# Optimization experiments

Hardware: AMD Instinct MI355X
Metric: run time of the kernel (lower is better)

## Reference

```python
import jax, jax.numpy as jnp
import numpy as np

N = 100000      # nodes
E = 1600000     # edges (avg degree 16)
IN = 256        # in_dim
OUT = 64        # out_dim per head
H = 4           # num_heads
SLOPE = 0.01    # F.leaky_relu default negative_slope


def setup_inputs() -> dict:
    key = jax.random.key(0)
    k1, k2, k3, k4, k5 = jax.random.split(key, 5)
    h = jax.random.normal(k1, (N, IN), dtype=jnp.float32)
    # per-head projection Linear(in_dim, out_dim, bias=False): weight [OUT, IN]
    W = jax.random.normal(k2, (H, OUT, IN), dtype=jnp.float32) * (1.0 / np.sqrt(IN))
    # per-head attention Linear(2*out_dim, 1, bias=False): weight flattened to [2*OUT]
    attn = jax.random.normal(k3, (H, 2 * OUT), dtype=jnp.float32) * (1.0 / np.sqrt(2 * OUT))
    edge_src = jax.random.randint(k4, (E,), 0, N, dtype=jnp.int32)
    edge_dst = jax.random.randint(k5, (E,), 0, N, dtype=jnp.int32)
    return {"h": h, "W": W, "attn": attn, "edge_src": edge_src, "edge_dst": edge_dst}


def reference(h, W, attn, edge_src, edge_dst):
    # Bug-faithful: edge_attention always uses self.heads[0][1], i.e. head 0's
    # attention vector, for every head.
    a0 = attn[0]                      # [2*OUT]
    a_src, a_dst = a0[:OUT], a0[OUT:]
    outs = []
    for hd in range(H):               # fixed small structural loop over heads
        z = h @ W[hd].T               # [N, OUT]
        # concat(z_src, z_dst) @ a0 == z_src @ a_src + z_dst @ a_dst
        s_src = z @ a_src             # [N]
        s_dst = z @ a_dst             # [N]
        e = jax.nn.leaky_relu(s_src[edge_src] + s_dst[edge_dst], SLOPE)  # [E]
        # segment softmax over incoming edges of each destination node
        m = jax.ops.segment_max(e, edge_dst, num_segments=N)
        m = jnp.where(jnp.isfinite(m), m, 0.0)   # guard zero-in-degree nodes
        ex = jnp.exp(e - m[edge_dst])
        den = jax.ops.segment_sum(ex, edge_dst, num_segments=N)
        alpha = ex / jnp.maximum(den[edge_dst], 1e-9)          # [E]
        msg = alpha[:, None] * z[edge_src]                      # [E, OUT]
        outs.append(jax.ops.segment_sum(msg, edge_dst, num_segments=N))  # [N, OUT]
    return jnp.concatenate(outs, axis=1)  # merge='cat' -> [N, H*OUT]
```

## Files before the change

kernel.cpp:

```cpp
#include <hip/hip_runtime.h>

#define K_IN   256
#define C_OUT  256
#define HEADS  4
#define PAD    64
#define BKT    256
#define REP    16
#define CAP    448

typedef __attribute__((ext_vector_type(8))) short s16x8;
typedef __attribute__((ext_vector_type(4))) short s16x4;
typedef __attribute__((ext_vector_type(4))) float f32x4;
typedef __attribute__((ext_vector_type(4))) int   i32x4;

static __device__ __forceinline__ unsigned short f2bf(float f) {
  union { float f; unsigned u; } v; v.f = f;
  unsigned r = v.u + 0x7FFFu + ((v.u >> 16) & 1u);
  return (unsigned short)(r >> 16);
}
static __device__ __forceinline__ float bf2f(unsigned short u) {
  union { unsigned u; float f; } v; v.u = (unsigned)u << 16;
  return v.f;
}
static __device__ __forceinline__ unsigned cvt_pk_bf16(float lo, float hi) {
  unsigned r;
  asm volatile("v_cvt_pk_bf16_f32 %0, %1, %2" : "=v"(r) : "v"(lo), "v"(hi));
  return r;
}
static __device__ __forceinline__ float fast_exp2(float x) {
  float r;
  asm("v_exp_f32 %0, %1" : "=v"(r) : "v"(x));
  return r;
}

__global__ void cvt_w(const float* __restrict__ Wm, unsigned short* __restrict__ Wf) {
  int idx = blockIdx.x * blockDim.x + threadIdx.x;
  if (idx >= 65536) return;
  int j    = idx & 7;
  int lane = (idx >> 3) & 63;
  int s    = (idx >> 9) & 3;
  int ks   = (idx >> 11) & 7;
  int cb   = (idx >> 14) & 3;
  int c = cb * 64 + s * 16 + (lane & 15);
  int k = ks * 32 + (lane >> 4) * 8 + j;
  Wf[idx] = f2bf(Wm[c * K_IN + k]);
}

static __device__ __forceinline__ void gemm_body(int bid,
    const float* __restrict__ h, const unsigned short* __restrict__ Wf,
    const float* __restrict__ attn, unsigned short* __restrict__ zb,
    float* __restrict__ ssrc, float* __restrict__ sdst, int n_nodes) {
  const int wv   = threadIdx.x >> 6;
  const int lane = threadIdx.x & 63;
  const int l15  = lane & 15;
  const int lhi  = lane >> 4;
  const int r0   = bid * 64 + wv * 16;

  f32x4 acc[16];
#pragma unroll
  for (int f = 0; f < 16; ++f) acc[f] = (f32x4){0.f, 0.f, 0.f, 0.f};

  int n = r0 + l15;
  if (n > n_nodes - 1) n = n_nodes - 1;
  const long long arow = (long long)n * K_IN;
  const int kbase = lhi * 8;

#pragma unroll
  for (int ks = 0; ks < 8; ++ks) {
    const int k = ks * 32 + kbase;
    const float4* pa = reinterpret_cast<const float4*>(h + arow + k);
    float4 v0 = pa[0], v1 = pa[1];
    union { s16x8 v; unsigned u[4]; } au;
    au.u[0] = cvt_pk_bf16(v0.x, v0.y);
    au.u[1] = cvt_pk_bf16(v0.z, v0.w);
    au.u[2] = cvt_pk_bf16(v1.x, v1.y);
    au.u[3] = cvt_pk_bf16(v1.z, v1.w);
    s16x8 a = au.v;
#pragma unroll
    for (int f = 0; f < 16; ++f) {
      s16x8 b = *reinterpret_cast<const s16x8*>(
          Wf + (((f >> 2) * 8 + ks) * 4 + (f & 3)) * 512 + lane * 8);
      acc[f] = __builtin_amdgcn_mfma_f32_16x16x32_bf16(a, b, acc[f], 0, 0, 0);
    }
  }

#pragma unroll
  for (int reg = 0; reg < 4; ++reg) {
    int row = r0 + lhi * 4 + reg;
    if (row < n_nodes) {
#pragma unroll
      for (int f = 0; f < 16; ++f)
        zb[(size_t)row * C_OUT + f * 16 + l15] = f2bf(acc[f][reg]);
    }
  }

  const float LOG2E = 1.4426950408889634f;
  float as_[4], ad_[4];
#pragma unroll
  for (int s = 0; s < 4; ++s) {
    as_[s] = attn[s * 16 + l15];
    ad_[s] = attn[64 + s * 16 + l15];
  }
#pragma unroll
  for (int reg = 0; reg < 4; ++reg) {
    int row = r0 + lhi * 4 + reg;
    float ps[4], pd[4];
#pragma unroll
    for (int hd = 0; hd < 4; ++hd) {
      ps[hd] = acc[hd * 4 + 0][reg] * as_[0] + acc[hd * 4 + 1][reg] * as_[1] +
               acc[hd * 4 + 2][reg] * as_[2] + acc[hd * 4 + 3][reg] * as_[3];
      pd[hd] = acc[hd * 4 + 0][reg] * ad_[0] + acc[hd * 4 + 1][reg] * ad_[1] +
               acc[hd * 4 + 2][reg] * ad_[2] + acc[hd * 4 + 3][reg] * ad_[3];
#pragma unroll
      for (int d = 1; d < 16; d <<= 1) {
        ps[hd] += __shfl_xor(ps[hd], d, 64);
        pd[hd] += __shfl_xor(pd[hd], d, 64);
      }
    }
    if (l15 == 0 && row < n_nodes) {
#pragma unroll
      for (int hd = 0; hd < 4; ++hd) {
        ssrc[(size_t)row * 4 + hd] = ps[hd] * LOG2E;
        sdst[(size_t)row * 4 + hd] = pd[hd] * LOG2E;
      }
    }
  }
}

static __device__ __forceinline__ void scatter_body(int sbid,
    const int* __restrict__ src, const int* __restrict__ dst, int E,
    int* __restrict__ cursors, int* __restrict__ stage) {
  int i = sbid * 256 + threadIdx.x;
  int rep = sbid & (REP - 1);
  int e4 = E >> 2;
  if (i < e4) {
    i32x4 d = __builtin_nontemporal_load(reinterpret_cast<const i32x4*>(dst) + i);
    i32x4 s = __builtin_nontemporal_load(reinterpret_cast<const i32x4*>(src) + i);
#pragma unroll
    for (int k = 0; k < 4; ++k) {
      int c = (d[k] >> 8) * REP + rep;
      int p = atomicAdd(&cursors[c], 1);
      if (p < CAP) stage[c * CAP + p] = (s[k] << 8) | (d[k] & 255);
    }
  }
  if (i < (E & 3)) {
    int j = (e4 << 2) + i;
    int dd = dst[j], ss = src[j];
    int c = (dd >> 8) * REP + rep;
    int p = atomicAdd(&cursors[c], 1);
    if (p < CAP) stage[c * CAP + p] = (ss << 8) | (dd & 255);
  }
}

__global__ __launch_bounds__(256) void gemm_scatter(
    const float* __restrict__ h, const unsigned short* __restrict__ Wf,
    const float* __restrict__ attn, unsigned short* __restrict__ zb,
    float* __restrict__ ssrc, float* __restrict__ sdst, int n_nodes,
    int g_gemm, const int* __restrict__ e_src, const int* __restrict__ e_dst,
    int E, int g_scat, int* __restrict__ cursors, int* __restrict__ stage) {
  int bid = blockIdx.x;
  if ((bid & 1) == 0) {
    int g = bid >> 1;
    if (g < g_gemm)
      gemm_body(g, h, Wf, attn, zb, ssrc, sdst, n_nodes);
  } else {
    int s = bid >> 1;
    if (s < g_scat)
      scatter_body(s, e_src, e_dst, E, cursors, stage);
  }
}

__global__ __launch_bounds__(256) void scatter_r2(const int* __restrict__ cursors,
                                                  const int* __restrict__ stage,
                                                  int N, int* __restrict__ counts,
                                                  int* __restrict__ csrp) {
  int b = blockIdx.x;
  int base = b << 8;
  __shared__ int cnt[BKT];
  for (int i = threadIdx.x; i < BKT; i += 256) cnt[i] = 0;
  __syncthreads();
  for (int rep = 0; rep < REP; ++rep) {
    int c = b * REP + rep;
    int len = min(cursors[c], CAP);
    for (int j = threadIdx.x; j < len; j += 256) {
      int v = stage[c * CAP + j];
      int d = v & 255, s = v >> 8;
      int slot = atomicAdd(&cnt[d], 1);
      if (slot < PAD) csrp[(size_t)(base + d) * PAD + slot] = s;
    }
  }
  __syncthreads();
  for (int i = threadIdx.x; i < BKT; i += 256) {
    int n = base + i;
    if (n < N) counts[n] = min(cnt[i], PAD);
  }
}

__global__ void scatter_pad(const int* __restrict__ src, const int* __restrict__ dst,
                            int e, int* __restrict__ cursor, int* __restrict__ csrp) {
  int i = blockIdx.x * blockDim.x + threadIdx.x;
  int e4 = e >> 2;
  if (i < e4) {
    i32x4 d = __builtin_nontemporal_load(reinterpret_cast<const i32x4*>(dst) + i);
    i32x4 s = __builtin_nontemporal_load(reinterpret_cast<const i32x4*>(src) + i);
#pragma unroll
    for (int k = 0; k < 4; ++k) {
      int p = atomicAdd(&cursor[d[k]], 1);
      csrp[d[k] * PAD + p] = s[k];
    }
  }
  if (i < (e & 3)) {
    int j = (e4 << 2) + i;
    int p = atomicAdd(&cursor[dst[j]], 1);
    csrp[dst[j] * PAD + p] = src[j];
  }
}

__global__ __launch_bounds__(256) void aggregate(const unsigned short* __restrict__ zb,
                                                 const float* __restrict__ ssrc,
                                                 const float* __restrict__ sdst,
                                                 const int* __restrict__ cnts,
                                                 const int* __restrict__ csr,
                                                 float* __restrict__ out,
                                                 int n0, int n1) {
  int w = n0 + blockIdx.x * (blockDim.x >> 6) + (threadIdx.x >> 6);
  if (w >= n1) return;
  int lane = threadIdx.x & 63;
  int head = lane >> 4;
  int beg = w * PAD;
  int end = beg + cnts[w];
  float sd = sdst[(size_t)w * 4 + head];
  float ax = 0.f, ay = 0.f, az = 0.f, aw = 0.f;
  float den = 0.f;
  for (int e = beg; e < end; e += 8) {
    int srcs[8];
#pragma unroll
    for (int j = 0; j < 8; ++j) {
      int idx = e + j;
      if (idx >= end) idx = end - 1;
      srcs[j] = __builtin_nontemporal_load(csr + idx);
    }
    float ss[8];
#pragma unroll
    for (int j = 0; j < 8; ++j)
      ss[j] = ssrc[(size_t)srcs[j] * 4 + head];
    s16x4 zv[8];
#pragma unroll
    for (int j = 0; j < 8; ++j)
      zv[j] = *reinterpret_cast<const s16x4*>(zb + (size_t)srcs[j] * C_OUT + lane * 4);
#pragma unroll
    for (int j = 0; j < 8; ++j) {
      float x = ss[j] + sd;
      x = x > 0.f ? x : 0.01f * x;
      float ex = fast_exp2(x);
      ex = (e + j < end) ? ex : 0.f;
      den += ex;
      ax += ex * bf2f((unsigned short)zv[j][0]);
      ay += ex * bf2f((unsigned short)zv[j][1]);
      az += ex * bf2f((unsigned short)zv[j][2]);
      aw += ex * bf2f((unsigned short)zv[j][3]);
    }
  }
  float inv = (end > beg) ? 1.f / fmaxf(den, 1e-9f) : 0.f;
  f32x4 o = {ax * inv, ay * inv, az * inv, aw * inv};
  __builtin_nontemporal_store(o, reinterpret_cast<f32x4*>(out + (size_t)w * C_OUT + lane * 4));
}

extern "C" void kernel_launch(void* const* d_in, const int* in_sizes, int n_in,
                              void* d_out, int out_size, void* d_ws, size_t ws_size,
                              hipStream_t stream) {
  const float* h    = (const float*)d_in[0];
  const float* Wm   = (const float*)d_in[1];
  const float* attn = (const float*)d_in[2];
  const int* e_src  = (const int*)d_in[3];
  const int* e_dst  = (const int*)d_in[4];
  float* out = (float*)d_out;

  const int N = in_sizes[0] / K_IN;
  const int E = in_sizes[3];
  const int NBK = (N + BKT - 1) / BKT;

  char* p = (char*)d_ws;
  unsigned short* zb = (unsigned short*)p; p += (size_t)N * C_OUT * sizeof(unsigned short);
  float* ssrc = (float*)p; p += (size_t)N * HEADS * sizeof(float);
  float* sdst = (float*)p; p += (size_t)N * HEADS * sizeof(float);
  int* counts = (int*)p;   p += (size_t)N * sizeof(int);
  unsigned short* Wf = (unsigned short*)p; p += 65536 * sizeof(unsigned short);
  int* csrp   = (int*)p;   p += (size_t)N * PAD * sizeof(int);
  int* cursors = (int*)p;  p += (size_t)NBK * REP * sizeof(int);
  int* stage   = (int*)p;
  const size_t need_binned = (size_t)(p - (char*)d_ws) + (size_t)NBK * REP * CAP * sizeof(int);
  const bool binned = ws_size >= need_binned;

  const int g_gemm = (N + 63) / 64;
  const int g_scat = ((E >> 2) + 255) / 256;

  hipLaunchKernelGGL(cvt_w, dim3(256), dim3(256), 0, stream, Wm, Wf);

  if (binned) {
    (void)hipMemsetAsync(cursors, 0, (size_t)NBK * REP * sizeof(int), stream);
    const int gmax = (g_gemm > g_scat ? g_gemm : g_scat);
    hipLaunchKernelGGL(gemm_scatter, dim3(2 * gmax), dim3(256), 0, stream,
                       h, Wf, attn, zb, ssrc, sdst, N, g_gemm,
                       e_src, e_dst, E, g_scat, cursors, stage);
    hipLaunchKernelGGL(scatter_r2, dim3(NBK), dim3(256), 0, stream,
                       cursors, stage, N, counts, csrp);
  } else {
    hipLaunchKernelGGL(gemm_scatter, dim3(2 * g_gemm), dim3(256), 0, stream,
                       h, Wf, attn, zb, ssrc, sdst, N, g_gemm,
                       e_src, e_dst, 0, 0, (int*)nullptr, (int*)nullptr);
    (void)hipMemsetAsync(counts, 0, (size_t)N * sizeof(int), stream);
    hipLaunchKernelGGL(scatter_pad, dim3(g_scat), dim3(256), 0, stream,
                       e_src, e_dst, E, counts, csrp);
  }

  const int half = N / 2;
  hipLaunchKernelGGL(aggregate, dim3((half + 3) / 4), dim3(256), 0, stream,
                     zb, ssrc, sdst, counts, csrp, out, 0, half);
  hipLaunchKernelGGL(aggregate, dim3((N - half + 3) / 4), dim3(256), 0, stream,
                     zb, ssrc, sdst, counts, csrp, out, half, N);
}
```

Before: 271.1 us.

## Rebalance fused GEMM/scatter blocks 3:1 and batch loads for more memory parallelism

Changes the block interleaving in the fused gemm_scatter kernel from 1:1 to three GEMM blocks per scatter block. Each scatter block now handles four times as many edges, issuing all loads up front and then batching the atomics. The GEMM hoists all 16 weight-fragment loads ahead of the MFMA chain, and launch_bounds(256,2) is added. The aim is to cut the grid-wide idle blocks and raise memory-level parallelism, at the cost of higher register pressure and possible changes to occupancy and atomic contention.

```diff
diff --git a/kernel.cpp b/kernel.cpp
--- a/kernel.cpp
+++ b/kernel.cpp
@@ -70,6 +70,11 @@
     const int k = ks * 32 + kbase;
     const float4* pa = reinterpret_cast<const float4*>(h + arow + k);
     float4 v0 = pa[0], v1 = pa[1];
+    s16x8 b[16];
+#pragma unroll
+    for (int f = 0; f < 16; ++f)
+      b[f] = *reinterpret_cast<const s16x8*>(
+          Wf + (((f >> 2) * 8 + ks) * 4 + (f & 3)) * 512 + lane * 8);
     union { s16x8 v; unsigned u[4]; } au;
     au.u[0] = cvt_pk_bf16(v0.x, v0.y);
     au.u[1] = cvt_pk_bf16(v0.z, v0.w);
@@ -77,11 +82,8 @@
     au.u[3] = cvt_pk_bf16(v1.z, v1.w);
     s16x8 a = au.v;
 #pragma unroll
-    for (int f = 0; f < 16; ++f) {
-      s16x8 b = *reinterpret_cast<const s16x8*>(
-          Wf + (((f >> 2) * 8 + ks) * 4 + (f & 3)) * 512 + lane * 8);
-      acc[f] = __builtin_amdgcn_mfma_f32_16x16x32_bf16(a, b, acc[f], 0, 0, 0);
-    }
+    for (int f = 0; f < 16; ++f)
+      acc[f] = __builtin_amdgcn_mfma_f32_16x16x32_bf16(a, b[f], acc[f], 0, 0, 0);
   }
 
 #pragma unroll
@@ -130,21 +132,34 @@
 static __device__ __forceinline__ void scatter_body(int sbid,
     const int* __restrict__ src, const int* __restrict__ dst, int E,
     int* __restrict__ cursors, int* __restrict__ stage) {
-  int i = sbid * 256 + threadIdx.x;
-  int rep = sbid & (REP - 1);
-  int e4 = E >> 2;
-  if (i < e4) {
-    i32x4 d = __builtin_nontemporal_load(reinterpret_cast<const i32x4*>(dst) + i);
-    i32x4 s = __builtin_nontemporal_load(reinterpret_cast<const i32x4*>(src) + i);
-#pragma unroll
-    for (int k = 0; k < 4; ++k) {
-      int c = (d[k] >> 8) * REP + rep;
-      int p = atomicAdd(&cursors[c], 1);
-      if (p < CAP) stage[c * CAP + p] = (s[k] << 8) | (d[k] & 255);
-    }
-  }
-  if (i < (E & 3)) {
-    int j = (e4 << 2) + i;
+  const int rep = sbid & (REP - 1);
+  const int e4 = E >> 2;
+  const int base = sbid * 1024 + threadIdx.x;
+  i32x4 d[4], s[4];
+  int have[4];
+#pragma unroll
+  for (int q = 0; q < 4; ++q) {
+    int idx = base + q * 256;
+    have[q] = (idx < e4);
+    int cidx = have[q] ? idx : (e4 > 0 ? e4 - 1 : 0);
+    d[q] = __builtin_nontemporal_load(reinterpret_cast<const i32x4*>(dst) + cidx);
+    s[q] = __builtin_nontemporal_load(reinterpret_cast<const i32x4*>(src) + cidx);
+  }
+#pragma unroll
+  for (int q = 0; q < 4; ++q) {
+    if (have[q]) {
+      int p0 = atomicAdd(&cursors[(d[q][0] >> 8) * REP + rep], 1);
+      int p1 = atomicAdd(&cursors[(d[q][1] >> 8) * REP + rep], 1);
+      int p2 = atomicAdd(&cursors[(d[q][2] >> 8) * REP + rep], 1);
+      int p3 = atomicAdd(&cursors[(d[q][3] >> 8) * REP + rep], 1);
+      if (p0 < CAP) stage[((d[q][0] >> 8) * REP + rep) * CAP + p0] = (s[q][0] << 8) | (d[q][0] & 255);
+      if (p1 < CAP) stage[((d[q][1] >> 8) * REP + rep) * CAP + p1] = (s[q][1] << 8) | (d[q][1] & 255);
+      if (p2 < CAP) stage[((d[q][2] >> 8) * REP + rep) * CAP + p2] = (s[q][2] << 8) | (d[q][2] & 255);
+      if (p3 < CAP) stage[((d[q][3] >> 8) * REP + rep) * CAP + p3] = (s[q][3] << 8) | (d[q][3] & 255);
+    }
+  }
+  if (sbid == 0 && threadIdx.x < (E & 3)) {
+    int j = (e4 << 2) + threadIdx.x;
     int dd = dst[j], ss = src[j];
     int c = (dd >> 8) * REP + rep;
     int p = atomicAdd(&cursors[c], 1);
@@ -152,19 +167,20 @@
   }
 }
 
-__global__ __launch_bounds__(256) void gemm_scatter(
+__global__ __launch_bounds__(256, 2) void gemm_scatter(
     const float* __restrict__ h, const unsigned short* __restrict__ Wf,
     const float* __restrict__ attn, unsigned short* __restrict__ zb,
     float* __restrict__ ssrc, float* __restrict__ sdst, int n_nodes,
     int g_gemm, const int* __restrict__ e_src, const int* __restrict__ e_dst,
     int E, int g_scat, int* __restrict__ cursors, int* __restrict__ stage) {
   int bid = blockIdx.x;
-  if ((bid & 1) == 0) {
-    int g = bid >> 1;
+  int slot = bid & 3;
+  if (slot < 3) {
+    int g = (bid >> 2) * 3 + slot;
     if (g < g_gemm)
       gemm_body(g, h, Wf, attn, zb, ssrc, sdst, n_nodes);
   } else {
-    int s = bid >> 1;
+    int s = bid >> 2;
     if (s < g_scat)
       scatter_body(s, e_src, e_dst, E, cursors, stage);
   }
@@ -293,24 +309,26 @@
   const bool binned = ws_size >= need_binned;
 
   const int g_gemm = (N + 63) / 64;
-  const int g_scat = ((E >> 2) + 255) / 256;
+  const int g_scat = ((E >> 2) + 1023) / 1024;
 
   hipLaunchKernelGGL(cvt_w, dim3(256), dim3(256), 0, stream, Wm, Wf);
 
   if (binned) {
     (void)hipMemsetAsync(cursors, 0, (size_t)NBK * REP * sizeof(int), stream);
-    const int gmax = (g_gemm > g_scat ? g_gemm : g_scat);
-    hipLaunchKernelGGL(gemm_scatter, dim3(2 * gmax), dim3(256), 0, stream,
+    int groups = (g_gemm + 2) / 3;
+    if (groups < g_scat) groups = g_scat;
+    hipLaunchKernelGGL(gemm_scatter, dim3(4 * groups), dim3(256), 0, stream,
                        h, Wf, attn, zb, ssrc, sdst, N, g_gemm,
                        e_src, e_dst, E, g_scat, cursors, stage);
     hipLaunchKernelGGL(scatter_r2, dim3(NBK), dim3(256), 0, stream,
                        cursors, stage, N, counts, csrp);
   } else {
-    hipLaunchKernelGGL(gemm_scatter, dim3(2 * g_gemm), dim3(256), 0, stream,
+    int groups = (g_gemm + 2) / 3;
+    hipLaunchKernelGGL(gemm_scatter, dim3(4 * groups), dim3(256), 0, stream,
                        h, Wf, attn, zb, ssrc, sdst, N, g_gemm,
                        e_src, e_dst, 0, 0, (int*)nullptr, (int*)nullptr);
     (void)hipMemsetAsync(counts, 0, (size_t)N * sizeof(int), stream);
-    hipLaunchKernelGGL(scatter_pad, dim3(g_scat), dim3(256), 0, stream,
+    hipLaunchKernelGGL(scatter_pad, dim3(((E >> 2) + 255) / 256), dim3(256), 0, stream,
                        e_src, e_dst, E, counts, csrp);
   }
 
```

New measurement: 291.7 us. 1.08x slower.

## Double GEMM rows per wave to reuse W fragments and rebalance block interleave

Applied to the files above, without the earlier changes.

Each wave now computes two 16-row tiles, so every loaded W fragment feeds two MFMAs, and each block covers 128 nodes instead of 64. The fused launch interleaves one GEMM block with two scatter blocks in groups of three, matching the halved GEMM grid. This cuts W reads from L2/L1 per output row, at the cost of doubling accumulator registers (128 VGPRs of acc), which may lower occupancy or cause spills.

```diff
diff --git a/kernel.cpp b/kernel.cpp
--- a/kernel.cpp
+++ b/kernel.cpp
@@ -54,43 +54,44 @@
   const int lane = threadIdx.x & 63;
   const int l15  = lane & 15;
   const int lhi  = lane >> 4;
-  const int r0   = bid * 64 + wv * 16;
-
-  f32x4 acc[16];
-#pragma unroll
-  for (int f = 0; f < 16; ++f) acc[f] = (f32x4){0.f, 0.f, 0.f, 0.f};
-
-  int n = r0 + l15;
-  if (n > n_nodes - 1) n = n_nodes - 1;
-  const long long arow = (long long)n * K_IN;
+  const int r0   = bid * 128 + wv * 32;
+
+  f32x4 acc[2][16];
+#pragma unroll
+  for (int g = 0; g < 2; ++g)
+#pragma unroll
+    for (int f = 0; f < 16; ++f) acc[g][f] = (f32x4){0.f, 0.f, 0.f, 0.f};
+
+  long long arow[2];
+#pragma unroll
+  for (int g = 0; g < 2; ++g) {
+    int n = r0 + g * 16 + l15;
+    if (n > n_nodes - 1) n = n_nodes - 1;
+    arow[g] = (long long)n * K_IN;
+  }
   const int kbase = lhi * 8;
 
 #pragma unroll
   for (int ks = 0; ks < 8; ++ks) {
     const int k = ks * 32 + kbase;
-    const float4* pa = reinterpret_cast<const float4*>(h + arow + k);
-    float4 v0 = pa[0], v1 = pa[1];
-    union { s16x8 v; unsigned u[4]; } au;
-    au.u[0] = cvt_pk_bf16(v0.x, v0.y);
-    au.u[1] = cvt_pk_bf16(v0.z, v0.w);
-    au.u[2] = cvt_pk_bf16(v1.x, v1.y);
-    au.u[3] = cvt_pk_bf16(v1.z, v1.w);
-    s16x8 a = au.v;
+    s16x8 a[2];
+#pragma unroll
+    for (int g = 0; g < 2; ++g) {
+      const float4* pa = reinterpret_cast<const float4*>(h + arow[g] + k);
+      float4 v0 = pa[0], v1 = pa[1];
+      union { s16x8 v; unsigned u[4]; } au;
+      au.u[0] = cvt_pk_bf16(v0.x, v0.y);
+      au.u[1] = cvt_pk_bf16(v0.z, v0.w);
+      au.u[2] = cvt_pk_bf16(v1.x, v1.y);
+      au.u[3] = cvt_pk_bf16(v1.z, v1.w);
+      a[g] = au.v;
+    }
 #pragma unroll
     for (int f = 0; f < 16; ++f) {
       s16x8 b = *reinterpret_cast<const s16x8*>(
           Wf + (((f >> 2) * 8 + ks) * 4 + (f & 3)) * 512 + lane * 8);
-      acc[f] = __builtin_amdgcn_mfma_f32_16x16x32_bf16(a, b, acc[f], 0, 0, 0);
-    }
-  }
-
-#pragma unroll
-  for (int reg = 0; reg < 4; ++reg) {
-    int row = r0 + lhi * 4 + reg;
-    if (row < n_nodes) {
-#pragma unroll
-      for (int f = 0; f < 16; ++f)
-        zb[(size_t)row * C_OUT + f * 16 + l15] = f2bf(acc[f][reg]);
+      acc[0][f] = __builtin_amdgcn_mfma_f32_16x16x32_bf16(a[0], b, acc[0][f], 0, 0, 0);
+      acc[1][f] = __builtin_amdgcn_mfma_f32_16x16x32_bf16(a[1], b, acc[1][f], 0, 0, 0);
     }
   }
 
@@ -101,27 +102,36 @@
     as_[s] = attn[s * 16 + l15];
     ad_[s] = attn[64 + s * 16 + l15];
   }
-#pragma unroll
-  for (int reg = 0; reg < 4; ++reg) {
-    int row = r0 + lhi * 4 + reg;
-    float ps[4], pd[4];
-#pragma unroll
-    for (int hd = 0; hd < 4; ++hd) {
-      ps[hd] = acc[hd * 4 + 0][reg] * as_[0] + acc[hd * 4 + 1][reg] * as_[1] +
-               acc[hd * 4 + 2][reg] * as_[2] + acc[hd * 4 + 3][reg] * as_[3];
-      pd[hd] = acc[hd * 4 + 0][reg] * ad_[0] + acc[hd * 4 + 1][reg] * ad_[1] +
-               acc[hd * 4 + 2][reg] * ad_[2] + acc[hd * 4 + 3][reg] * ad_[3];
-#pragma unroll
-      for (int d = 1; d < 16; d <<= 1) {
-        ps[hd] += __shfl_xor(ps[hd], d, 64);
-        pd[hd] += __shfl_xor(pd[hd], d, 64);
+
+#pragma unroll
+  for (int g = 0; g < 2; ++g) {
+#pragma unroll
+    for (int reg = 0; reg < 4; ++reg) {
+      int row = r0 + g * 16 + lhi * 4 + reg;
+      if (row < n_nodes) {
+#pragma unroll
+        for (int f = 0; f < 16; ++f)
+          zb[(size_t)row * C_OUT + f * 16 + l15] = f2bf(acc[g][f][reg]);
       }
-    }
-    if (l15 == 0 && row < n_nodes) {
+      float ps[4], pd[4];
 #pragma unroll
       for (int hd = 0; hd < 4; ++hd) {
-        ssrc[(size_t)row * 4 + hd] = ps[hd] * LOG2E;
-        sdst[(size_t)row * 4 + hd] = pd[hd] * LOG2E;
+        ps[hd] = acc[g][hd * 4 + 0][reg] * as_[0] + acc[g][hd * 4 + 1][reg] * as_[1] +
+                 acc[g][hd * 4 + 2][reg] * as_[2] + acc[g][hd * 4 + 3][reg] * as_[3];
+        pd[hd] = acc[g][hd * 4 + 0][reg] * ad_[0] + acc[g][hd * 4 + 1][reg] * ad_[1] +
+                 acc[g][hd * 4 + 2][reg] * ad_[2] + acc[g][hd * 4 + 3][reg] * ad_[3];
+#pragma unroll
+        for (int d = 1; d < 16; d <<= 1) {
+          ps[hd] += __shfl_xor(ps[hd], d, 64);
+          pd[hd] += __shfl_xor(pd[hd], d, 64);
+        }
+      }
+      if (l15 == 0 && row < n_nodes) {
+#pragma unroll
+        for (int hd = 0; hd < 4; ++hd) {
+          ssrc[(size_t)row * 4 + hd] = ps[hd] * LOG2E;
+          sdst[(size_t)row * 4 + hd] = pd[hd] * LOG2E;
+        }
       }
     }
   }
@@ -159,12 +169,13 @@
     int g_gemm, const int* __restrict__ e_src, const int* __restrict__ e_dst,
     int E, int g_scat, int* __restrict__ cursors, int* __restrict__ stage) {
   int bid = blockIdx.x;
-  if ((bid & 1) == 0) {
-    int g = bid >> 1;
-    if (g < g_gemm)
-      gemm_body(g, h, Wf, attn, zb, ssrc, sdst, n_nodes);
+  int grp = bid / 3;
+  int slot = bid - grp * 3;
+  if (slot == 0) {
+    if (grp < g_gemm)
+      gemm_body(grp, h, Wf, attn, zb, ssrc, sdst, n_nodes);
   } else {
-    int s = bid >> 1;
+    int s = grp * 2 + (slot - 1);
     if (s < g_scat)
       scatter_body(s, e_src, e_dst, E, cursors, stage);
   }
@@ -292,21 +303,23 @@
   const size_t need_binned = (size_t)(p - (char*)d_ws) + (size_t)NBK * REP * CAP * sizeof(int);
   const bool binned = ws_size >= need_binned;
 
-  const int g_gemm = (N + 63) / 64;
+  const int g_gemm = (N + 127) / 128;
   const int g_scat = ((E >> 2) + 255) / 256;
 
   hipLaunchKernelGGL(cvt_w, dim3(256), dim3(256), 0, stream, Wm, Wf);
 
   if (binned) {
     (void)hipMemsetAsync(cursors, 0, (size_t)NBK * REP * sizeof(int), stream);
-    const int gmax = (g_gemm > g_scat ? g_gemm : g_scat);
-    hipLaunchKernelGGL(gemm_scatter, dim3(2 * gmax), dim3(256), 0, stream,
+    int groups = g_gemm;
+    int need_s = (g_scat + 1) / 2;
+    if (groups < need_s) groups = need_s;
+    hipLaunchKernelGGL(gemm_scatter, dim3(3 * groups), dim3(256), 0, stream,
                        h, Wf, attn, zb, ssrc, sdst, N, g_gemm,
                        e_src, e_dst, E, g_scat, cursors, stage);
     hipLaunchKernelGGL(scatter_r2, dim3(NBK), dim3(256), 0, stream,
                        cursors, stage, N, counts, csrp);
   } else {
-    hipLaunchKernelGGL(gemm_scatter, dim3(2 * g_gemm), dim3(256), 0, stream,
+    hipLaunchKernelGGL(gemm_scatter, dim3(3 * g_gemm), dim3(256), 0, stream,
                        h, Wf, attn, zb, ssrc, sdst, N, g_gemm,
                        e_src, e_dst, 0, 0, (int*)nullptr, (int*)nullptr);
     (void)hipMemsetAsync(counts, 0, (size_t)N * sizeof(int), stream);
```

After: 276.3 us. No clear change (+1.9%).

## Stage bf16 weight slices in double-buffered LDS for the fused GEMM

Applied to the files above, without the earlier changes.

Reorders the converted weight layout so each k-step slice is contiguous, then has the block cooperatively load it into a double-buffered shared-memory tile. The next slice is prefetched into registers while the MFMAs run. Previously each wave read its B fragments from global/L2 on its own. This adds 32KB of LDS per block to the fused gemm/scatter kernel, including the scatter blocks, which can lower occupancy. It also adds a barrier per k-step.

```diff
diff --git a/kernel.cpp b/kernel.cpp
--- a/kernel.cpp
+++ b/kernel.cpp
@@ -33,25 +33,27 @@
   return r;
 }
 
-__global__ void cvt_w(const float* __restrict__ Wm, unsigned short* __restrict__ Wf) {
+__global__ void cvt_w(const float* __restrict__ Wm, unsigned short* __restrict__ Wf2) {
   int idx = blockIdx.x * blockDim.x + threadIdx.x;
   if (idx >= 65536) return;
   int j    = idx & 7;
   int lane = (idx >> 3) & 63;
   int s    = (idx >> 9) & 3;
-  int ks   = (idx >> 11) & 7;
-  int cb   = (idx >> 14) & 3;
+  int cb   = (idx >> 11) & 3;
+  int ks   = (idx >> 13) & 7;
   int c = cb * 64 + s * 16 + (lane & 15);
   int k = ks * 32 + (lane >> 4) * 8 + j;
-  Wf[idx] = f2bf(Wm[c * K_IN + k]);
+  Wf2[idx] = f2bf(Wm[c * K_IN + k]);
 }
 
 static __device__ __forceinline__ void gemm_body(int bid,
-    const float* __restrict__ h, const unsigned short* __restrict__ Wf,
+    const float* __restrict__ h, const unsigned short* __restrict__ Wf2,
     const float* __restrict__ attn, unsigned short* __restrict__ zb,
-    float* __restrict__ ssrc, float* __restrict__ sdst, int n_nodes) {
-  const int wv   = threadIdx.x >> 6;
-  const int lane = threadIdx.x & 63;
+    float* __restrict__ ssrc, float* __restrict__ sdst, int n_nodes,
+    s16x8 (*lds_b)[1024]) {
+  const int tid  = threadIdx.x;
+  const int wv   = tid >> 6;
+  const int lane = tid & 63;
   const int l15  = lane & 15;
   const int lhi  = lane >> 4;
   const int r0   = bid * 64 + wv * 16;
@@ -65,8 +67,22 @@
   const long long arow = (long long)n * K_IN;
   const int kbase = lhi * 8;
 
+  {
+    const s16x8* src = reinterpret_cast<const s16x8*>(Wf2);
+#pragma unroll
+    for (int r = 0; r < 4; ++r) lds_b[0][tid + r * 256] = src[tid + r * 256];
+  }
+  __syncthreads();
+
 #pragma unroll
   for (int ks = 0; ks < 8; ++ks) {
+    const int cur = ks & 1;
+    s16x8 st[4];
+    if (ks < 7) {
+      const s16x8* src = reinterpret_cast<const s16x8*>(Wf2 + (ks + 1) * 8192);
+#pragma unroll
+      for (int r = 0; r < 4; ++r) st[r] = src[tid + r * 256];
+    }
     const int k = ks * 32 + kbase;
     const float4* pa = reinterpret_cast<const float4*>(h + arow + k);
     float4 v0 = pa[0], v1 = pa[1];
@@ -78,9 +94,13 @@
     s16x8 a = au.v;
 #pragma unroll
     for (int f = 0; f < 16; ++f) {
-      s16x8 b = *reinterpret_cast<const s16x8*>(
-          Wf + (((f >> 2) * 8 + ks) * 4 + (f & 3)) * 512 + lane * 8);
+      s16x8 b = lds_b[cur][f * 64 + lane];
       acc[f] = __builtin_amdgcn_mfma_f32_16x16x32_bf16(a, b, acc[f], 0, 0, 0);
+    }
+    if (ks < 7) {
+#pragma unroll
+      for (int r = 0; r < 4; ++r) lds_b[cur ^ 1][tid + r * 256] = st[r];
+      __syncthreads();
     }
   }
 
@@ -153,16 +173,17 @@
 }
 
 __global__ __launch_bounds__(256) void gemm_scatter(
-    const float* __restrict__ h, const unsigned short* __restrict__ Wf,
+    const float* __restrict__ h, const unsigned short* __restrict__ Wf2,
     const float* __restrict__ attn, unsigned short* __restrict__ zb,
     float* __restrict__ ssrc, float* __restrict__ sdst, int n_nodes,
     int g_gemm, const int* __restrict__ e_src, const int* __restrict__ e_dst,
     int E, int g_scat, int* __restrict__ cursors, int* __restrict__ stage) {
+  __shared__ s16x8 lds_b[2][1024];
   int bid = blockIdx.x;
   if ((bid & 1) == 0) {
     int g = bid >> 1;
     if (g < g_gemm)
-      gemm_body(g, h, Wf, attn, zb, ssrc, sdst, n_nodes);
+      gemm_body(g, h, Wf2, attn, zb, ssrc, sdst, n_nodes, lds_b);
   } else {
     int s = bid >> 1;
     if (s < g_scat)
@@ -285,7 +306,7 @@
   float* ssrc = (float*)p; p += (size_t)N * HEADS * sizeof(float);
   float* sdst = (float*)p; p += (size_t)N * HEADS * sizeof(float);
   int* counts = (int*)p;   p += (size_t)N * sizeof(int);
-  unsigned short* Wf = (unsigned short*)p; p += 65536 * sizeof(unsigned short);
+  unsigned short* Wf2 = (unsigned short*)p; p += 65536 * sizeof(unsigned short);
   int* csrp   = (int*)p;   p += (size_t)N * PAD * sizeof(int);
   int* cursors = (int*)p;  p += (size_t)NBK * REP * sizeof(int);
   int* stage   = (int*)p;
@@ -295,19 +316,19 @@
   const int g_gemm = (N + 63) / 64;
   const int g_scat = ((E >> 2) + 255) / 256;
 
-  hipLaunchKernelGGL(cvt_w, dim3(256), dim3(256), 0, stream, Wm, Wf);
+  hipLaunchKernelGGL(cvt_w, dim3(256), dim3(256), 0, stream, Wm, Wf2);
 
   if (binned) {
     (void)hipMemsetAsync(cursors, 0, (size_t)NBK * REP * sizeof(int), stream);
     const int gmax = (g_gemm > g_scat ? g_gemm : g_scat);
     hipLaunchKernelGGL(gemm_scatter, dim3(2 * gmax), dim3(256), 0, stream,
-                       h, Wf, attn, zb, ssrc, sdst, N, g_gemm,
+                       h, Wf2, attn, zb, ssrc, sdst, N, g_gemm,
                        e_src, e_dst, E, g_scat, cursors, stage);
     hipLaunchKernelGGL(scatter_r2, dim3(NBK), dim3(256), 0, stream,
                        cursors, stage, N, counts, csrp);
   } else {
     hipLaunchKernelGGL(gemm_scatter, dim3(2 * g_gemm), dim3(256), 0, stream,
-                       h, Wf, attn, zb, ssrc, sdst, N, g_gemm,
+                       h, Wf2, attn, zb, ssrc, sdst, N, g_gemm,
                        e_src, e_dst, 0, 0, (int*)nullptr, (int*)nullptr);
     (void)hipMemsetAsync(counts, 0, (size_t)N * sizeof(int), stream);
     hipLaunchKernelGGL(scatter_pad, dim3(g_scat), dim3(256), 0, stream,
```

Result: faster. 258.8 us (-4.5%).
